# Kernel tuning notes

Measured on AMD Instinct MI355X. Metric: run time of the kernel, lower is better.

Reference implementation:

```python
import jax, jax.numpy as jnp
import numpy as np

E = 512        # embedding_dim
DM = 512       # d_model
H = 8          # num_heads
HD = DM // H   # head_dim
NL = 4         # (e_num_layers-1) + (d_num_layers-1) identical VaeEncoder blocks
CIN = 32       # input_dim
EPS = 1e-5


def setup_inputs() -> dict:
    key = jax.random.key(0)
    ks = jax.random.split(key, 8)
    s = 0.02
    n = lambda k, shape: jax.random.normal(k, shape, jnp.float32) * s
    return {
        "x": jax.random.normal(ks[0], (4, 2048, CIN), jnp.float32),
        "conv_w": n(ks[1], (E, CIN, 3)),
        "conv_b": jnp.zeros((E,), jnp.float32),
        "qkv_w": n(ks[2], (NL, 3 * DM, E)),
        "qkv_b": jnp.zeros((NL, 3 * DM), jnp.float32),
        "out_w": n(ks[3], (NL, E, DM)),
        "out_b": jnp.zeros((NL, E), jnp.float32),
        "fc1_w": n(ks[4], (NL, E, E)),
        "fc1_b": jnp.zeros((NL, E), jnp.float32),
        "fc2_w": n(ks[5], (NL, E, E)),
        "fc2_b": jnp.zeros((NL, E), jnp.float32),
        "ln1_w": jnp.ones((NL, E), jnp.float32),
        "ln1_b": jnp.zeros((NL, E), jnp.float32),
        "ln2_w": jnp.ones((NL, E), jnp.float32),
        "ln2_b": jnp.zeros((NL, E), jnp.float32),
        "outp_w": n(ks[6], (CIN, E)),
        "outp_b": jnp.zeros((CIN,), jnp.float32),
    }


def _pos_embedding(L, d):
    pos = jnp.arange(L, dtype=jnp.float32)[:, None]
    div = jnp.exp(jnp.arange(0, d, 2, dtype=jnp.float32) * (-np.log(10000.0) / d))
    pe = jnp.zeros((L, d), jnp.float32)
    pe = pe.at[:, 0::2].set(jnp.sin(pos * div))
    pe = pe.at[:, 1::2].set(jnp.cos(pos * div))
    return pe


def _layernorm(x, w, b):
    mu = jnp.mean(x, axis=-1, keepdims=True)
    xc = x - mu
    inv = jax.lax.rsqrt(jnp.mean(xc * xc, axis=-1, keepdims=True) + EPS)
    return xc * inv * w + b


def _encoder_block(x, p):
    (qkv_w, qkv_b, out_w, out_b, fc1_w, fc1_b, fc2_w, fc2_b,
     ln1_w, ln1_b, ln2_w, ln2_b) = p
    B, L, _ = x.shape
    qkv = x @ qkv_w.T + qkv_b                      # [B, L, 3*DM]
    q = qkv[:, :, :DM].reshape(B, L, H, HD)
    k = qkv[:, :, DM:2 * DM].reshape(B, L, H, HD)
    v = qkv[:, :, 2 * DM:].reshape(B, L, H, HD)
    scores = jnp.einsum('bqhd,bkhd->bhqk', q, k)   # [B, H, L, L]
    attn = jax.nn.softmax(scores / jnp.sqrt(jnp.float32(HD)), axis=-1)
    ctx = jnp.einsum('bhqk,bkhd->bqhd', attn, v).reshape(B, L, DM)
    x = _layernorm(x + (ctx @ out_w.T + out_b), ln1_w, ln1_b)
    h = jax.nn.silu(x @ fc1_w.T + fc1_b) @ fc2_w.T + fc2_b
    return _layernorm(x + h, ln2_w, ln2_b)


def reference(x, conv_w, conv_b, qkv_w, qkv_b, out_w, out_b,
              fc1_w, fc1_b, fc2_w, fc2_b, ln1_w, ln1_b, ln2_w, ln2_b,
              outp_w, outp_b):
    B, L, _ = x.shape
    # TokenEmbedding: circular Conv1d k=3 pad=1 over the time axis
    xc = jnp.pad(x.transpose(0, 2, 1), ((0, 0), (0, 0), (1, 1)), mode='wrap')
    h = jax.lax.conv_general_dilated(
        xc, conv_w, (1,), 'VALID',
        dimension_numbers=('NCH', 'OIH', 'NCH')) + conv_b[None, :, None]
    h = h.transpose(0, 2, 1) + _pos_embedding(L, E)[None]
    params = (qkv_w, qkv_b, out_w, out_b, fc1_w, fc1_b, fc2_w, fc2_b,
              ln1_w, ln1_b, ln2_w, ln2_b)
    def step(carry, p):
        return _encoder_block(carry, p), None
    h, _ = jax.lax.scan(step, h, params)
    return h @ outp_w.T + outp_b
```

## Files before the change

kernel.cpp:

```cpp
#include <hip/hip_runtime.h>
#include <hip/hip_bf16.h>
#include <cstddef>

typedef short bf16x8 __attribute__((ext_vector_type(8)));
typedef float f32x4 __attribute__((ext_vector_type(4)));

__device__ __forceinline__ unsigned short f2bf(float x) {
  __hip_bfloat16 h = __float2bfloat16(x);
  unsigned short u; __builtin_memcpy(&u, &h, 2); return u;
}
__device__ __forceinline__ float bf2f(unsigned short u) {
  unsigned int v = ((unsigned int)u) << 16; float f; __builtin_memcpy(&f, &v, 4); return f;
}
__device__ __forceinline__ float swz16f(float x) {
  int i; __builtin_memcpy(&i, &x, 4);
  i = __builtin_amdgcn_ds_swizzle(i, 0x401F);
  float r; __builtin_memcpy(&r, &i, 4); return r;
}
__device__ __forceinline__ void gload16(const unsigned short* g, unsigned short* l) {
  __builtin_amdgcn_global_load_lds(
      (const __attribute__((address_space(1))) void*)g,
      (__attribute__((address_space(3))) void*)l, 16, 0, 0);
}
__device__ __forceinline__ void pipe_sync() {
  asm volatile("s_waitcnt vmcnt(0)" ::: "memory");
  __builtin_amdgcn_s_barrier();
  __builtin_amdgcn_sched_barrier(0);
}
__device__ __forceinline__ void bar_only() {
  asm volatile("" ::: "memory");
  __builtin_amdgcn_s_barrier();
  __builtin_amdgcn_sched_barrier(0);
}

__global__ __launch_bounds__(256) void cvt_all(
    const float* __restrict__ qkv_w, const float* __restrict__ out_w,
    const float* __restrict__ fc1_w, const float* __restrict__ fc2_w,
    const float* __restrict__ outp_w, unsigned short* __restrict__ dst)
{
  int i = blockIdx.x * 256 + threadIdx.x;
  if (i >= 1576960) return;
  const float* src; int off;
  if (i < 786432)       { src = qkv_w;  off = i; }
  else if (i < 1048576) { src = out_w;  off = i - 786432; }
  else if (i < 1310720) { src = fc1_w;  off = i - 1048576; }
  else if (i < 1572864) { src = fc2_w;  off = i - 1310720; }
  else                  { src = outp_w; off = i - 1572864; }
  float4 v = *(const float4*)(src + (size_t)off * 4);
  ushort4 o;
  o.x = f2bf(v.x); o.y = f2bf(v.y); o.z = f2bf(v.z); o.w = f2bf(v.w);
  *(ushort4*)(dst + (size_t)i * 4) = o;
}

__global__ __launch_bounds__(256) void conv_pe_kernel(
    const float* __restrict__ x, const float* __restrict__ cw,
    const float* __restrict__ cb, unsigned short* __restrict__ outb)
{
  const int L = 2048;
  int b  = blockIdx.x >> 8;
  int l0 = (blockIdx.x & 255) << 3;
  int t  = threadIdx.x;
  __shared__ __align__(16) float xs[10][32];
  for (int idx = t; idx < 320; idx += 256) {
    int rr = idx >> 5, ci = idx & 31;
    int gl = (l0 - 1 + rr + L) & (L - 1);
    xs[rr][ci] = x[((size_t)b * L + gl) * 32 + ci];
  }
  __syncthreads();
  int e0 = t << 1;
  float acc0[8], acc1[8];
  float bb0 = cb[e0], bb1 = cb[e0 + 1];
#pragma unroll
  for (int li = 0; li < 8; li++) { acc0[li] = bb0; acc1[li] = bb1; }

  const float4* w04 = (const float4*)(cw + (size_t)e0 * 96);
  const float4* w14 = (const float4*)(cw + (size_t)e0 * 96 + 96);

#pragma unroll
  for (int c4 = 0; c4 < 8; c4++) {
    float4 wa0 = w04[3 * c4], wa1 = w04[3 * c4 + 1], wa2 = w04[3 * c4 + 2];
    float4 wb0 = w14[3 * c4], wb1 = w14[3 * c4 + 1], wb2 = w14[3 * c4 + 2];
    float w0v[12] = {wa0.x, wa0.y, wa0.z, wa0.w, wa1.x, wa1.y, wa1.z, wa1.w,
                     wa2.x, wa2.y, wa2.z, wa2.w};
    float w1v[12] = {wb0.x, wb0.y, wb0.z, wb0.w, wb1.x, wb1.y, wb1.z, wb1.w,
                     wb2.x, wb2.y, wb2.z, wb2.w};
    float4 xr[10];
#pragma unroll
    for (int r = 0; r < 10; r++) xr[r] = *(const float4*)&xs[r][c4 * 4];
#pragma unroll
    for (int li = 0; li < 8; li++) {
#pragma unroll
      for (int kk = 0; kk < 3; kk++) {
        float4 xv = xr[li + kk];
        acc0[li] += xv.x * w0v[kk] + xv.y * w0v[3 + kk]
                  + xv.z * w0v[6 + kk] + xv.w * w0v[9 + kk];
        acc1[li] += xv.x * w1v[kk] + xv.y * w1v[3 + kk]
                  + xv.z * w1v[6 + kk] + xv.w * w1v[9 + kk];
      }
    }
  }

  float dv = __expf((float)e0 * (-9.210340371976184f / 512.0f));
#pragma unroll
  for (int li = 0; li < 8; li++) {
    int l = l0 + li;
    float arg = (float)l * dv;
    float sv = __sinf(arg), cv = __cosf(arg);
    size_t off = ((size_t)b * L + l) * 512 + e0;
    ushort2 ob; ob.x = f2bf(acc0[li] + sv); ob.y = f2bf(acc1[li] + cv);
    *(ushort2*)&outb[off] = ob;
  }
}

template<int EPI, int QSCALE, int NFR, int VOUT>
__global__ __launch_bounds__(256) void gemm_bf(
    const unsigned short* __restrict__ X,
    const unsigned short* __restrict__ W,
    const float* __restrict__ bias,
    const unsigned short* __restrict__ R,
    unsigned short* __restrict__ Yb,
    float* __restrict__ Yf,
    unsigned short* __restrict__ VT,
    int N)
{
  const int K = 512;
  constexpr int BN = NFR * 32;
  constexpr int WB = NFR * 4096;
  constexpr int BUF = 16384 + WB;
  __shared__ __align__(16) char smem[2 * BUF];
  int t = threadIdx.x;
  int lane = t & 63, wv = t >> 6;
  int g = lane >> 4, li = lane & 15;
  int m0 = (blockIdx.x & 63) << 7;
  int n0 = (blockIdx.x >> 6) * BN;
  int wm = (wv >> 1) << 6;
  int wn = (wv & 1) * (BN / 2);

  int subrow = lane >> 3;
  int coloff = ((lane & 7) ^ subrow) << 3;

  f32x4 acc[4][NFR];
#pragma unroll
  for (int a = 0; a < 4; a++)
#pragma unroll
    for (int b2 = 0; b2 < NFR; b2++) acc[a][b2] = (f32x4){0.f, 0.f, 0.f, 0.f};

#pragma unroll
  for (int j = 0; j < 4; j++) {
    int row = (wv * 4 + j) * 8 + subrow;
    gload16(X + (size_t)(m0 + row) * K + coloff,
            (unsigned short*)(smem + (wv * 4 + j) * 1024));
  }
#pragma unroll
  for (int j = 0; j < NFR; j++) {
    int row = (wv * NFR + j) * 8 + subrow;
    gload16(W + (size_t)(n0 + row) * K + coloff,
            (unsigned short*)(smem + 16384 + (wv * NFR + j) * 1024));
  }

#pragma unroll
  for (int ks = 0; ks < 8; ks++) {
    const int buf = ks & 1;
    char* cur = smem + buf * BUF;
    if (ks < 7) {
      char* nxt = smem + (buf ^ 1) * BUF;
      int k0 = (ks + 1) * 64;
#pragma unroll
      for (int j = 0; j < 4; j++) {
        int row = (wv * 4 + j) * 8 + subrow;
        gload16(X + (size_t)(m0 + row) * K + k0 + coloff,
                (unsigned short*)(nxt + (wv * 4 + j) * 1024));
      }
#pragma unroll
      for (int j = 0; j < NFR; j++) {
        int row = (wv * NFR + j) * 8 + subrow;
        gload16(W + (size_t)(n0 + row) * K + k0 + coloff,
                (unsigned short*)(nxt + 16384 + (wv * NFR + j) * 1024));
      }
      if constexpr (NFR == 4) asm volatile("s_waitcnt vmcnt(8)" ::: "memory");
      else if constexpr (NFR == 2) asm volatile("s_waitcnt vmcnt(6)" ::: "memory");
      else asm volatile("s_waitcnt vmcnt(5)" ::: "memory");
    } else {
      asm volatile("s_waitcnt vmcnt(0)" ::: "memory");
    }
    __builtin_amdgcn_s_barrier();
    __builtin_amdgcn_sched_barrier(0);

#pragma unroll
    for (int s = 0; s < 2; s++) {
      bf16x8 af[4], bfr[NFR];
#pragma unroll
      for (int mt = 0; mt < 4; mt++) {
        int row = wm + 16 * mt + li;
        af[mt] = *(const bf16x8*)(cur + (row * 8 + ((g + 4 * s) ^ (row & 7))) * 16);
      }
#pragma unroll
      for (int nt = 0; nt < NFR; nt++) {
        int row = wn + 16 * nt + li;
        bfr[nt] = *(const bf16x8*)(cur + 16384 +
                                   (row * 8 + ((g + 4 * s) ^ (row & 7))) * 16);
      }
#pragma unroll
      for (int mt = 0; mt < 4; mt++)
#pragma unroll
        for (int nt = 0; nt < NFR; nt++)
          acc[mt][nt] = __builtin_amdgcn_mfma_f32_16x16x32_bf16(
              af[mt], bfr[nt], acc[mt][nt], 0, 0, 0);
    }
    if (ks < 7) bar_only();
  }

  float bv[NFR];
#pragma unroll
  for (int nt = 0; nt < NFR; nt++) bv[nt] = bias[n0 + wn + 16 * nt + li];

  if (VOUT && n0 >= 1024) {
    unsigned short* Ts = (unsigned short*)smem;
    __builtin_amdgcn_s_barrier();
#pragma unroll
    for (int nt = 0; nt < NFR; nt++) {
      int col = wn + 16 * nt + li;
      float bvn = bv[nt];
#pragma unroll
      for (int mt = 0; mt < 4; mt++) {
        float v0 = acc[mt][nt][0] + bvn, v1 = acc[mt][nt][1] + bvn;
        float v2 = acc[mt][nt][2] + bvn, v3 = acc[mt][nt][3] + bvn;
        uint2 pk;
        asm("v_cvt_pk_bf16_f32 %0, %1, %2" : "=v"(pk.x) : "v"(v0), "v"(v1));
        asm("v_cvt_pk_bf16_f32 %0, %1, %2" : "=v"(pk.y) : "v"(v2), "v"(v3));
        *(uint2*)(Ts + col * 136 + wm + 16 * mt + 4 * g) = pk;
      }
    }
    __syncthreads();
    int vcol = t >> 1, half = t & 1;
    int gc = n0 - 1024 + vcol;
    int bh = (m0 >> 11) * 8 + (gc >> 6);
    int d  = gc & 63;
    unsigned short* dst = VT + ((size_t)bh * 64 + d) * 2048 + (m0 & 2047) + half * 64;
    const unsigned short* srcp = Ts + vcol * 136 + half * 64;
#pragma unroll
    for (int j2 = 0; j2 < 8; j2++)
      *(bf16x8*)(dst + j2 * 8) = *(const bf16x8*)(srcp + j2 * 8);
    return;
  }

#pragma unroll
  for (int mt = 0; mt < 4; mt++) {
#pragma unroll
    for (int i = 0; i < 4; i++) {
      size_t roff = (size_t)(m0 + wm + 16 * mt + 4 * g + i) * N;
#pragma unroll
      for (int nt = 0; nt < NFR; nt++) {
        int col = n0 + wn + 16 * nt + li;
        float v = acc[mt][nt][i] + bv[nt];
        if (EPI == 1) {
          v += bf2f(R[roff + col]);
          Yb[roff + col] = f2bf(v);
        } else if (EPI == 2) {
          v = v / (1.f + __expf(-v));
          Yb[roff + col] = f2bf(v);
        } else if (EPI == 3) {
          Yf[roff + col] = v;
        } else {
          if (QSCALE && col < 512) v *= 0.18033688011112042f;
          Yb[roff + col] = f2bf(v);
        }
      }
    }
  }
}

__global__ __launch_bounds__(256) void attn_mfma(
    const unsigned short* __restrict__ qkv,
    const unsigned short* __restrict__ Vt,
    unsigned short* __restrict__ ctx)
{
  const int L = 2048;
  int bh = blockIdx.x & 31, qi = blockIdx.x >> 5;
  int b = bh >> 3, h = bh & 7;
  int q0 = qi << 7;
  size_t tb = (size_t)b * L;
  int t = threadIdx.x, lane = t & 63, wv = t >> 6;
  int g = lane >> 4, li = lane & 15;
  int lisw7 = li & 7;

  __shared__ __align__(16) char smem[65536];

  int wq = q0 + wv * 32;
  bf16x8 qf00, qf01, qf10, qf11;
  {
    const unsigned short* qp0 = qkv + (tb + wq + li) * 1536 + h * 64 + g * 8;
    qf00 = *(const bf16x8*)qp0;
    qf01 = *(const bf16x8*)(qp0 + 32);
    const unsigned short* qp1 = qp0 + (size_t)16 * 1536;
    qf10 = *(const bf16x8*)qp1;
    qf11 = *(const bf16x8*)(qp1 + 32);
  }

  f32x4 accA[4], accB[4];
#pragma unroll
  for (int nt = 0; nt < 4; nt++) {
    accA[nt] = (f32x4){0.f, 0.f, 0.f, 0.f};
    accB[nt] = (f32x4){0.f, 0.f, 0.f, 0.f};
  }
  float lA = 0.f, lB = 0.f;

  int rowE = ((li >> 2) << 3) + (li & 3);
  int swzE = (li >> 2) << 1;
  int swzO = swzE + 1;
  int kE0 = rowE * 128 + ((g ^ swzE) << 4);
  int kE1 = rowE * 128 + (((g + 4) ^ swzE) << 4);
  int kO0 = (rowE + 4) * 128 + ((g ^ swzO) << 4);
  int kO1 = (rowE + 4) * 128 + (((g + 4) ^ swzO) << 4);
  int vrowb = 16384 + li * 256;
  int vsl[4];
#pragma unroll
  for (int c = 0; c < 4; c++) vsl[c] = ((g + 4 * c) ^ lisw7) << 4;

  int subrow = lane >> 3;
  const unsigned short* kp[4];
  const unsigned short* vp[4];
#pragma unroll
  for (int j = 0; j < 4; j++) {
    int krow = (wv * 4 + j) * 8 + subrow;
    int swzk = (2 * j + (subrow >> 2)) & 7;
    kp[j] = qkv + (tb + krow) * 1536 + 512 + h * 64 + (((lane & 7) ^ swzk) << 3);
    int vrow = (wv * 4 + j) * 4 + g;
    vp[j] = Vt + ((size_t)bh * 64 + vrow) * 2048 + ((li ^ (vrow & 7)) << 3);
  }

#pragma unroll
  for (int j = 0; j < 4; j++) {
    gload16(kp[j], (unsigned short*)(smem + (wv * 4 + j) * 1024));
    gload16(vp[j], (unsigned short*)(smem + 16384 + (wv * 4 + j) * 1024));
    kp[j] += (size_t)128 * 1536; vp[j] += 128;
  }
  pipe_sync();

#pragma unroll 2
  for (int it = 0; it < 16; it++) {
    const int buf = it & 1;
    const char* base = smem + buf * 32768;
    if (it < 15) {
      char* nb = smem + (buf ^ 1) * 32768;
#pragma unroll
      for (int j = 0; j < 4; j++) {
        gload16(kp[j], (unsigned short*)(nb + (wv * 4 + j) * 1024));
        gload16(vp[j], (unsigned short*)(nb + 16384 + (wv * 4 + j) * 1024));
        kp[j] += (size_t)128 * 1536; vp[j] += 128;
      }
    }

    float psA = 0.f, psB = 0.f;
    const f32x4 kZ = {0.f, 0.f, 0.f, 0.f};
#pragma unroll
    for (int c = 0; c < 4; c++) {
      const char* cb_ = base + c * 4096;
      bf16x8 k0 = *(const bf16x8*)(cb_ + kE0);
      bf16x8 k1 = *(const bf16x8*)(cb_ + kE1);
      bf16x8 k2 = *(const bf16x8*)(cb_ + kO0);
      bf16x8 k3 = *(const bf16x8*)(cb_ + kO1);
      __builtin_amdgcn_s_setprio(1);
      f32x4 sEA = __builtin_amdgcn_mfma_f32_16x16x32_bf16(k0, qf00, kZ, 0, 0, 0);
      f32x4 sEB = __builtin_amdgcn_mfma_f32_16x16x32_bf16(k0, qf10, kZ, 0, 0, 0);
      f32x4 sOA = __builtin_amdgcn_mfma_f32_16x16x32_bf16(k2, qf00, kZ, 0, 0, 0);
      f32x4 sOB = __builtin_amdgcn_mfma_f32_16x16x32_bf16(k2, qf10, kZ, 0, 0, 0);
      sEA = __builtin_amdgcn_mfma_f32_16x16x32_bf16(k1, qf01, sEA, 0, 0, 0);
      sEB = __builtin_amdgcn_mfma_f32_16x16x32_bf16(k1, qf11, sEB, 0, 0, 0);
      sOA = __builtin_amdgcn_mfma_f32_16x16x32_bf16(k3, qf01, sOA, 0, 0, 0);
      sOB = __builtin_amdgcn_mfma_f32_16x16x32_bf16(k3, qf11, sOB, 0, 0, 0);
      __builtin_amdgcn_s_setprio(0);

      bf16x8 paA, paB;
#define EPACK(SE, SO, PS, PA)                                                 \
      {                                                                       \
        float e0 = SE[0], e1 = SE[1], e2 = SE[2], e3 = SE[3];                 \
        float o0 = SO[0], o1 = SO[1], o2 = SO[2], o3 = SO[3];                 \
        asm volatile("v_exp_f32 %0, %0\n\tv_exp_f32 %1, %1\n\t"               \
                     "v_exp_f32 %2, %2\n\tv_exp_f32 %3, %3\n\ts_nop 1"        \
                     : "+v"(e0), "+v"(e1), "+v"(e2), "+v"(e3));               \
        asm volatile("v_exp_f32 %0, %0\n\tv_exp_f32 %1, %1\n\t"               \
                     "v_exp_f32 %2, %2\n\tv_exp_f32 %3, %3\n\ts_nop 1"        \
                     : "+v"(o0), "+v"(o1), "+v"(o2), "+v"(o3));               \
        PS += ((e0 + e1) + (e2 + e3)) + ((o0 + o1) + (o2 + o3));              \
        unsigned int d0, d1, d2, d3;                                          \
        asm("v_cvt_pk_bf16_f32 %0, %1, %2" : "=v"(d0) : "v"(e0), "v"(e1));    \
        asm("v_cvt_pk_bf16_f32 %0, %1, %2" : "=v"(d1) : "v"(e2), "v"(e3));    \
        asm("v_cvt_pk_bf16_f32 %0, %1, %2" : "=v"(d2) : "v"(o0), "v"(o1));    \
        asm("v_cvt_pk_bf16_f32 %0, %1, %2" : "=v"(d3) : "v"(o2), "v"(o3));    \
        unsigned int tmp_[4] = {d0, d1, d2, d3};                              \
        __builtin_memcpy(&PA, tmp_, 16);                                      \
      }
      EPACK(sEA, sOA, psA, paA)
      EPACK(sEB, sOB, psB, paB)
#undef EPACK

      __builtin_amdgcn_s_setprio(1);
#pragma unroll
      for (int nt = 0; nt < 4; nt++) {
        bf16x8 vb = *(const bf16x8*)(base + vrowb + nt * 4096 + vsl[c]);
        accA[nt] = __builtin_amdgcn_mfma_f32_16x16x32_bf16(paA, vb, accA[nt], 0, 0, 0);
        accB[nt] = __builtin_amdgcn_mfma_f32_16x16x32_bf16(paB, vb, accB[nt], 0, 0, 0);
      }
      __builtin_amdgcn_s_setprio(0);
    }

    psA += swz16f(psA); psA += __shfl_xor(psA, 32); lA += psA;
    psB += swz16f(psB); psB += __shfl_xor(psB, 32); lB += psB;

    pipe_sync();
  }

  float liA[4], liB[4];
#pragma unroll
  for (int i = 0; i < 4; i++) {
    liA[i] = 1.f / __shfl(lA, 4 * g + i);
    liB[i] = 1.f / __shfl(lB, 4 * g + i);
  }
#pragma unroll
  for (int i = 0; i < 4; i++) {
    size_t ra = (tb + wq + 4 * g + i) * 512 + h * 64;
    size_t rb = (tb + wq + 16 + 4 * g + i) * 512 + h * 64;
#pragma unroll
    for (int nt = 0; nt < 4; nt++) {
      ctx[ra + 16 * nt + li] = f2bf(accA[nt][i] * liA[i]);
      ctx[rb + 16 * nt + li] = f2bf(accB[nt][i] * liB[i]);
    }
  }
}

__global__ __launch_bounds__(256) void ln_kernel(
    const unsigned short* __restrict__ X, const float* __restrict__ g,
    const float* __restrict__ b, unsigned short* __restrict__ Yb)
{
  int t = threadIdx.x, lane = t & 63, wv = t >> 6;
  size_t row = (size_t)blockIdx.x * 4 + wv;
  bf16x8 xv = *(const bf16x8*)(X + row * 512 + lane * 8);
  float xf[8];
#pragma unroll
  for (int j = 0; j < 8; j++) xf[j] = bf2f((unsigned short)xv[j]);
  float sum = 0.f, sq = 0.f;
#pragma unroll
  for (int j = 0; j < 8; j++) { sum += xf[j]; sq += xf[j] * xf[j]; }
#pragma unroll
  for (int off = 32; off > 0; off >>= 1) {
    sum += __shfl_xor(sum, off);
    sq  += __shfl_xor(sq, off);
  }
  float mu  = sum * (1.0f / 512.0f);
  float inv = rsqrtf(sq * (1.0f / 512.0f) - mu * mu + 1e-5f);
  float4 g0 = *(const float4*)(g + lane * 8);
  float4 g1 = *(const float4*)(g + lane * 8 + 4);
  float4 b0 = *(const float4*)(b + lane * 8);
  float4 b1 = *(const float4*)(b + lane * 8 + 4);
  float gw[8] = {g0.x, g0.y, g0.z, g0.w, g1.x, g1.y, g1.z, g1.w};
  float bw[8] = {b0.x, b0.y, b0.z, b0.w, b1.x, b1.y, b1.z, b1.w};
  bf16x8 yb;
#pragma unroll
  for (int j = 0; j < 8; j++)
    yb[j] = (short)f2bf((xf[j] - mu) * inv * gw[j] + bw[j]);
  *(bf16x8*)(Yb + row * 512 + lane * 8) = yb;
}

extern "C" void kernel_launch(void* const* d_in, const int* in_sizes, int n_in,
                              void* d_out, int out_size, void* d_ws, size_t ws_size,
                              hipStream_t stream) {
  (void)in_sizes; (void)n_in; (void)out_size; (void)ws_size;
  const float* x      = (const float*)d_in[0];
  const float* conv_w = (const float*)d_in[1];
  const float* conv_b = (const float*)d_in[2];
  const float* qkv_w  = (const float*)d_in[3];
  const float* qkv_b  = (const float*)d_in[4];
  const float* out_w  = (const float*)d_in[5];
  const float* out_b  = (const float*)d_in[6];
  const float* fc1_w  = (const float*)d_in[7];
  const float* fc1_b  = (const float*)d_in[8];
  const float* fc2_w  = (const float*)d_in[9];
  const float* fc2_b  = (const float*)d_in[10];
  const float* ln1_w  = (const float*)d_in[11];
  const float* ln1_b  = (const float*)d_in[12];
  const float* ln2_w  = (const float*)d_in[13];
  const float* ln2_b  = (const float*)d_in[14];
  const float* outp_w = (const float*)d_in[15];
  const float* outp_b = (const float*)d_in[16];
  float* out = (float*)d_out;

  char* p = (char*)d_ws;
  unsigned short* A    = (unsigned short*)p;            p += (size_t)8192 * 512 * 2;
  unsigned short* QKV  = (unsigned short*)p;            p += (size_t)8192 * 1536 * 2;
  unsigned short* VT   = (unsigned short*)p;            p += (size_t)32 * 64 * 2048 * 2;
  unsigned short* CTX  = (unsigned short*)p;            p += (size_t)8192 * 512 * 2;
  unsigned short* Wq   = (unsigned short*)p;            p += (size_t)4 * 1536 * 512 * 2;
  unsigned short* Wo   = (unsigned short*)p;            p += (size_t)4 * 512 * 512 * 2;
  unsigned short* W1   = (unsigned short*)p;            p += (size_t)4 * 512 * 512 * 2;
  unsigned short* W2   = (unsigned short*)p;            p += (size_t)4 * 512 * 512 * 2;
  unsigned short* Wp   = (unsigned short*)p;            p += (size_t)32 * 512 * 2;
  unsigned short* D = QKV;

  cvt_all<<<6160, 256, 0, stream>>>(qkv_w, out_w, fc1_w, fc2_w, outp_w, Wq);

  conv_pe_kernel<<<1024, 256, 0, stream>>>(x, conv_w, conv_b, A);

  for (int l = 0; l < 4; l++) {
    gemm_bf<0, 1, 4, 1><<<64 * 12, 256, 0, stream>>>(
        A, Wq + (size_t)l * 1536 * 512, qkv_b + l * 1536, nullptr,
        QKV, nullptr, VT, 1536);
    attn_mfma<<<512, 256, 0, stream>>>(QKV, VT, CTX);
    gemm_bf<1, 0, 2, 0><<<64 * 8, 256, 0, stream>>>(
        CTX, Wo + (size_t)l * 512 * 512, out_b + l * 512, A,
        D, nullptr, nullptr, 512);
    ln_kernel<<<2048, 256, 0, stream>>>(D, ln1_w + l * 512, ln1_b + l * 512, A);
    gemm_bf<2, 0, 2, 0><<<64 * 8, 256, 0, stream>>>(
        A, W1 + (size_t)l * 512 * 512, fc1_b + l * 512, nullptr,
        CTX, nullptr, nullptr, 512);
    gemm_bf<1, 0, 2, 0><<<64 * 8, 256, 0, stream>>>(
        CTX, W2 + (size_t)l * 512 * 512, fc2_b + l * 512, A,
        D, nullptr, nullptr, 512);
    ln_kernel<<<2048, 256, 0, stream>>>(D, ln2_w + l * 512, ln2_b + l * 512, A);
  }
  gemm_bf<3, 0, 1, 0><<<64, 256, 0, stream>>>(
      A, Wp, outp_b, nullptr, nullptr, out, nullptr, 32);
}
```

Before: 464.3 us.

## Split attention over two key halves and combine partial results

Attention is split along the key dimension into two halves, which doubles the grid from 512 to 1024 blocks and halves the shared-memory tile per stage to 32 KB. Each half writes unnormalized fp32 accumulators and row sums to a workspace, and a new combine kernel adds the halves, normalizes and converts to bf16. The softmax has no running max, so the partial sums add directly. The aim is better occupancy and CU utilisation on the attention kernel. The cost is extra fp32 global traffic (about 32 MB written and read per layer) plus one more launch per layer.

```diff
diff --git a/kernel.cpp b/kernel.cpp
--- a/kernel.cpp
+++ b/kernel.cpp
@@ -273,18 +273,22 @@
 __global__ __launch_bounds__(256) void attn_mfma(
     const unsigned short* __restrict__ qkv,
     const unsigned short* __restrict__ Vt,
-    unsigned short* __restrict__ ctx)
+    float* __restrict__ Op,
+    float* __restrict__ Lp)
 {
   const int L = 2048;
-  int bh = blockIdx.x & 31, qi = blockIdx.x >> 5;
+  int bh = blockIdx.x & 31;
+  int rest = blockIdx.x >> 5;
+  int qi = rest & 15, half = rest >> 4;
   int b = bh >> 3, h = bh & 7;
   int q0 = qi << 7;
+  int kt0 = half << 10;
   size_t tb = (size_t)b * L;
   int t = threadIdx.x, lane = t & 63, wv = t >> 6;
   int g = lane >> 4, li = lane & 15;
   int lisw7 = li & 7;
 
-  __shared__ __align__(16) char smem[65536];
+  __shared__ __align__(16) char smem[32768];
 
   int wq = q0 + wv * 32;
   bf16x8 qf00, qf01, qf10, qf11;
@@ -312,49 +316,51 @@
   int kE1 = rowE * 128 + (((g + 4) ^ swzE) << 4);
   int kO0 = (rowE + 4) * 128 + ((g ^ swzO) << 4);
   int kO1 = (rowE + 4) * 128 + (((g + 4) ^ swzO) << 4);
-  int vrowb = 16384 + li * 256;
-  int vsl[4];
-#pragma unroll
-  for (int c = 0; c < 4; c++) vsl[c] = ((g + 4 * c) ^ lisw7) << 4;
+  int vrowb = 8192 + li * 128;
+  int vsl[2];
+#pragma unroll
+  for (int c = 0; c < 2; c++) vsl[c] = ((g + 4 * c) ^ lisw7) << 4;
 
   int subrow = lane >> 3;
-  const unsigned short* kp[4];
-  const unsigned short* vp[4];
-#pragma unroll
-  for (int j = 0; j < 4; j++) {
-    int krow = (wv * 4 + j) * 8 + subrow;
-    int swzk = (2 * j + (subrow >> 2)) & 7;
-    kp[j] = qkv + (tb + krow) * 1536 + 512 + h * 64 + (((lane & 7) ^ swzk) << 3);
-    int vrow = (wv * 4 + j) * 4 + g;
-    vp[j] = Vt + ((size_t)bh * 64 + vrow) * 2048 + ((li ^ (vrow & 7)) << 3);
-  }
-
-#pragma unroll
-  for (int j = 0; j < 4; j++) {
-    gload16(kp[j], (unsigned short*)(smem + (wv * 4 + j) * 1024));
-    gload16(vp[j], (unsigned short*)(smem + 16384 + (wv * 4 + j) * 1024));
-    kp[j] += (size_t)128 * 1536; vp[j] += 128;
+  const unsigned short* kp[2];
+  const unsigned short* vp[2];
+#pragma unroll
+  for (int j = 0; j < 2; j++) {
+    int krow = (wv * 2 + j) * 8 + subrow;
+    int swzk = ((wv & 1) * 4 + 2 * j + (subrow >> 2)) & 7;
+    kp[j] = qkv + (tb + kt0 + krow) * 1536 + 512 + h * 64
+            + (((lane & 7) ^ swzk) << 3);
+    int vrow = (wv * 2 + j) * 8 + subrow;
+    vp[j] = Vt + ((size_t)bh * 64 + vrow) * 2048 + kt0
+            + (((lane & 7) ^ (vrow & 7)) << 3);
+  }
+
+#pragma unroll
+  for (int j = 0; j < 2; j++) {
+    gload16(kp[j], (unsigned short*)(smem + (wv * 2 + j) * 1024));
+    gload16(vp[j], (unsigned short*)(smem + 8192 + (wv * 2 + j) * 1024));
+    kp[j] += (size_t)64 * 1536; vp[j] += 64;
   }
   pipe_sync();
 
 #pragma unroll 2
   for (int it = 0; it < 16; it++) {
     const int buf = it & 1;
-    const char* base = smem + buf * 32768;
+    const char* base = smem + buf * 16384;
     if (it < 15) {
-      char* nb = smem + (buf ^ 1) * 32768;
-#pragma unroll
-      for (int j = 0; j < 4; j++) {
-        gload16(kp[j], (unsigned short*)(nb + (wv * 4 + j) * 1024));
-        gload16(vp[j], (unsigned short*)(nb + 16384 + (wv * 4 + j) * 1024));
-        kp[j] += (size_t)128 * 1536; vp[j] += 128;
+      char* nb = smem + (buf ^ 1) * 16384;
+#pragma unroll
+      for (int j = 0; j < 2; j++) {
+        gload16(kp[j], (unsigned short*)(nb + (wv * 2 + j) * 1024));
+        gload16(vp[j], (unsigned short*)(nb + 8192 + (wv * 2 + j) * 1024));
+        kp[j] += (size_t)64 * 1536; vp[j] += 64;
       }
     }
 
     float psA = 0.f, psB = 0.f;
     const f32x4 kZ = {0.f, 0.f, 0.f, 0.f};
 #pragma unroll
-    for (int c = 0; c < 4; c++) {
+    for (int c = 0; c < 2; c++) {
       const char* cb_ = base + c * 4096;
       bf16x8 k0 = *(const bf16x8*)(cb_ + kE0);
       bf16x8 k1 = *(const bf16x8*)(cb_ + kE1);
@@ -398,7 +404,7 @@
       __builtin_amdgcn_s_setprio(1);
 #pragma unroll
       for (int nt = 0; nt < 4; nt++) {
-        bf16x8 vb = *(const bf16x8*)(base + vrowb + nt * 4096 + vsl[c]);
+        bf16x8 vb = *(const bf16x8*)(base + vrowb + nt * 2048 + vsl[c]);
         accA[nt] = __builtin_amdgcn_mfma_f32_16x16x32_bf16(paA, vb, accA[nt], 0, 0, 0);
         accB[nt] = __builtin_amdgcn_mfma_f32_16x16x32_bf16(paB, vb, accB[nt], 0, 0, 0);
       }
@@ -411,22 +417,47 @@
     pipe_sync();
   }
 
-  float liA[4], liB[4];
-#pragma unroll
-  for (int i = 0; i < 4; i++) {
-    liA[i] = 1.f / __shfl(lA, 4 * g + i);
-    liB[i] = 1.f / __shfl(lB, 4 * g + i);
-  }
+  float* Ob = Op + (size_t)half * 8192 * 512;
 #pragma unroll
   for (int i = 0; i < 4; i++) {
     size_t ra = (tb + wq + 4 * g + i) * 512 + h * 64;
     size_t rb = (tb + wq + 16 + 4 * g + i) * 512 + h * 64;
 #pragma unroll
     for (int nt = 0; nt < 4; nt++) {
-      ctx[ra + 16 * nt + li] = f2bf(accA[nt][i] * liA[i]);
-      ctx[rb + 16 * nt + li] = f2bf(accB[nt][i] * liB[i]);
-    }
-  }
+      Ob[ra + 16 * nt + li] = accA[nt][i];
+      Ob[rb + 16 * nt + li] = accB[nt][i];
+    }
+  }
+  if (g == 0) {
+    size_t lbase = ((size_t)(half * 8 + h)) * 8192;
+    Lp[lbase + tb + wq + li]      = lA;
+    Lp[lbase + tb + wq + 16 + li] = lB;
+  }
+}
+
+__global__ __launch_bounds__(256) void attn_combine(
+    const float* __restrict__ Op, const float* __restrict__ Lp,
+    unsigned short* __restrict__ ctx)
+{
+  int t = threadIdx.x, lane = t & 63, wv = t >> 6;
+  size_t row = (size_t)blockIdx.x * 4 + wv;
+  int h = lane >> 3;
+  float inv = 1.f / (Lp[(size_t)h * 8192 + row] +
+                     Lp[(size_t)(8 + h) * 8192 + row]);
+  const float* p1 = Op + row * 512 + lane * 8;
+  const float* p2 = p1 + (size_t)8192 * 512;
+  float4 a0 = *(const float4*)p1;
+  float4 a1 = *(const float4*)(p1 + 4);
+  float4 c0 = *(const float4*)p2;
+  float4 c1 = *(const float4*)(p2 + 4);
+  float vals[8] = {(a0.x + c0.x) * inv, (a0.y + c0.y) * inv,
+                   (a0.z + c0.z) * inv, (a0.w + c0.w) * inv,
+                   (a1.x + c1.x) * inv, (a1.y + c1.y) * inv,
+                   (a1.z + c1.z) * inv, (a1.w + c1.w) * inv};
+  bf16x8 o;
+#pragma unroll
+  for (int j = 0; j < 8; j++) o[j] = (short)f2bf(vals[j]);
+  *(bf16x8*)(ctx + row * 512 + lane * 8) = o;
 }
 
 __global__ __launch_bounds__(256) void ln_kernel(
@@ -495,6 +526,8 @@
   unsigned short* W1   = (unsigned short*)p;            p += (size_t)4 * 512 * 512 * 2;
   unsigned short* W2   = (unsigned short*)p;            p += (size_t)4 * 512 * 512 * 2;
   unsigned short* Wp   = (unsigned short*)p;            p += (size_t)32 * 512 * 2;
+  float*          OP   = (float*)p;                     p += (size_t)2 * 8192 * 512 * 4;
+  float*          LP   = (float*)p;                     p += (size_t)2 * 8 * 8192 * 4;
   unsigned short* D = QKV;
 
   cvt_all<<<6160, 256, 0, stream>>>(qkv_w, out_w, fc1_w, fc2_w, outp_w, Wq);
@@ -505,7 +538,8 @@
     gemm_bf<0, 1, 4, 1><<<64 * 12, 256, 0, stream>>>(
         A, Wq + (size_t)l * 1536 * 512, qkv_b + l * 1536, nullptr,
         QKV, nullptr, VT, 1536);
-    attn_mfma<<<512, 256, 0, stream>>>(QKV, VT, CTX);
+    attn_mfma<<<1024, 256, 0, stream>>>(QKV, VT, OP, LP);
+    attn_combine<<<2048, 256, 0, stream>>>(OP, LP, CTX);
     gemm_bf<1, 0, 2, 0><<<64 * 8, 256, 0, stream>>>(
         CTX, Wo + (size_t)l * 512 * 512, out_b + l * 512, A,
         D, nullptr, nullptr, 512);
```

Result: slower. 507.2 us (+9.2%).
